# Kernel tuning notes

Hardware: AMD Instinct MI355X
Metric: run time of the kernel (lower is better)

Reference implementation:

```python
import jax, jax.numpy as jnp
import numpy as np
import math

B, T, C = 4, 2048, 1024
N = 16
D = C // N  # 64
SCALE = 1.0 / math.sqrt(C)  # weight init scale, matches 1/sqrt(in_features)


def setup_inputs() -> dict:
    key = jax.random.key(0)
    ks = jax.random.split(key, 5)
    x = jax.random.normal(ks[0], (B, T, C), dtype=jnp.float32)
    wq = jax.random.normal(ks[1], (C, C), dtype=jnp.float32) * SCALE
    wk = jax.random.normal(ks[2], (C, C), dtype=jnp.float32) * SCALE
    wv = jax.random.normal(ks[3], (C, C), dtype=jnp.float32) * SCALE
    wp = jax.random.normal(ks[4], (C, C), dtype=jnp.float32) * SCALE
    zb = jnp.zeros((C,), dtype=jnp.float32)
    return {"x": x, "wq": wq, "bq": zb, "wk": wk, "bk": zb,
            "wv": wv, "bv": zb, "wp": wp, "bp": zb}


def reference(x, wq, bq, wk, bk, wv, bv, wp, bp):
    # q/k/v projections (torch Linear: x @ W.T + b), split into heads
    q = (x @ wq.T + bq).reshape(B, T, N, D)
    k = (x @ wk.T + bk).reshape(B, T, N, D)
    v = (x @ wv.T + bv).reshape(B, T, N, D)
    # scores [B, N, T, T] with causal mask (include_query=True -> key_dim = T)
    scores = jnp.einsum('bqnd,bknd->bnqk', q, k) / math.sqrt(D)
    causal = jnp.tril(jnp.ones((T, T), dtype=bool))
    scores = jnp.where(causal[None, None], scores, -jnp.inf)
    probs = jax.nn.softmax(scores, axis=-1)
    # attention output, clamp to [-10, 10] (drop_p = 0, head_mask = None)
    attn = jnp.einsum('bnqk,bknd->bqnd', probs, v)
    attn = jnp.clip(attn, -10.0, 10.0).reshape(B, T, C)
    out = attn @ wp.T + bp
    out = jnp.clip(out, -10.0, 10.0)
    return out
```

## Files before the change

### kernel.cpp

```cpp
#include <hip/hip_runtime.h>
#include <stdint.h>

typedef __attribute__((ext_vector_type(4))) float f32x4;
typedef __attribute__((ext_vector_type(8))) _Float16 h8;
typedef __attribute__((ext_vector_type(4))) float f4v;
typedef __attribute__((ext_vector_type(4))) _Float16 h4v;

#define B_ 4
#define T_ 2048
#define C_ 1024
#define NH 16
#define HD 64
#define M_ (B_*T_)
#define KD 1024

#define MFMA16(a, b, c) __builtin_amdgcn_mfma_f32_16x16x32_f16(a, b, c, 0, 0, 0)

#if __has_builtin(__builtin_amdgcn_exp2f)
#define EXP2(x) __builtin_amdgcn_exp2f(x)
#else
#define EXP2(x) exp2f(x)
#endif

#if __has_builtin(__builtin_amdgcn_cvt_pkrtz)
static __device__ __forceinline__ unsigned pk16(float a, float b) {
  return __builtin_bit_cast(unsigned, __builtin_amdgcn_cvt_pkrtz(a, b));
}
#else
static __device__ __forceinline__ unsigned pk16(float a, float b) {
  union { _Float16 h[2]; unsigned u; } x;
  x.h[0] = (_Float16)a; x.h[1] = (_Float16)b; return x.u;
}
#endif

#define GL2LDS16(g, l) \
  __builtin_amdgcn_global_load_lds((const __attribute__((address_space(1))) unsigned int*)(g), \
      (__attribute__((address_space(3))) unsigned int*)(unsigned int)(uintptr_t)(l), 16, 0, 0)

__global__ void cast_x_kernel(const float* __restrict__ src, _Float16* __restrict__ dst, int n4) {
  int i = blockIdx.x * blockDim.x + threadIdx.x;
  if (i < n4) {
    f4v v = ((const f4v*)src)[i];
    ((h4v*)dst)[i] = __builtin_convertvector(v, h4v);
  }
}

__device__ __forceinline__ void stage_f32_128x32(const float* src, _Float16* dst, int lane, int wav) {
  #pragma unroll
  for (int hh = 0; hh < 2; hh++) {
    int row = hh*64 + wav*16 + (lane >> 2);
    int colf = (lane & 3) * 8;
    const float* p = src + (size_t)row * KD + colf;
    f4v a = *(const f4v*)p;
    f4v b = *(const f4v*)(p + 4);
    h8 v;
    v[0]=(_Float16)a[0]; v[1]=(_Float16)a[1]; v[2]=(_Float16)a[2]; v[3]=(_Float16)a[3];
    v[4]=(_Float16)b[0]; v[5]=(_Float16)b[1]; v[6]=(_Float16)b[2]; v[7]=(_Float16)b[3];
    *(h8*)(dst + row*32 + colf) = v;
  }
}

template<int AMODE>
__global__ __launch_bounds__(256) void gemm_qkv_kernel(
    const _Float16* __restrict__ Xh, const float* __restrict__ Xf,
    const float* __restrict__ Wq, const float* __restrict__ Wk, const float* __restrict__ Wv,
    const float* __restrict__ bq, const float* __restrict__ bk, const float* __restrict__ bv,
    _Float16* __restrict__ Qo, _Float16* __restrict__ Ko, _Float16* __restrict__ Vo)
{
  __shared__ _Float16 As[128*32];
  __shared__ _Float16 Bs[128*32];
  int tid = threadIdx.x;
  int lane = tid & 63, wav = tid >> 6;
  int mb = blockIdx.x;
  int nbg = blockIdx.y;
  int sel = nbg >> 3, nb = nbg & 7;
  const float* W = sel == 0 ? Wq : (sel == 1 ? Wk : Wv);
  const float* bias = sel == 0 ? bq : (sel == 1 ? bk : bv);
  _Float16* Out = sel == 0 ? Qo : (sel == 1 ? Ko : Vo);
  int m0 = mb * 128, n0 = nb * 128;

  f32x4 acc[4][4] = {};

  int r_in = lane >> 2;
  int c8   = (lane & 3) * 8;
  int l15 = lane & 15, l4 = lane >> 4;
  int wr = (wav >> 1) * 64, wc = (wav & 1) * 64;

  for (int k0 = 0; k0 < KD; k0 += 32) {
    if (AMODE == 0) {
      GL2LDS16(Xh + (size_t)(m0 +      wav*16 + r_in)*KD + k0 + c8, As +        wav*512);
      GL2LDS16(Xh + (size_t)(m0 + 64 + wav*16 + r_in)*KD + k0 + c8, As + 2048 + wav*512);
    } else {
      stage_f32_128x32(Xf + (size_t)m0 * KD + k0, As, lane, wav);
    }
    stage_f32_128x32(W + (size_t)n0 * KD + k0, Bs, lane, wav);
    __syncthreads();

    h8 af[4], bf[4];
    #pragma unroll
    for (int f = 0; f < 4; f++) {
      af[f] = *(const h8*)(As + (wr + f*16 + l15)*32 + l4*8);
      bf[f] = *(const h8*)(Bs + (wc + f*16 + l15)*32 + l4*8);
    }
    #pragma unroll
    for (int i = 0; i < 4; i++)
      #pragma unroll
      for (int j = 0; j < 4; j++)
        acc[i][j] = MFMA16(af[i], bf[j], acc[i][j]);
    __syncthreads();
  }

  if (sel == 2) {
    #pragma unroll
    for (int i = 0; i < 4; i++) {
      int mrow = m0 + wr + i*16 + l4*4;
      int bb = mrow >> 11, t = mrow & 2047;
      #pragma unroll
      for (int j = 0; j < 4; j++) {
        int ncol = n0 + wc + j*16 + l15;
        float bval = bias[ncol];
        int hh = ncol >> 6, d = ncol & 63;
        h4v v;
        #pragma unroll
        for (int r = 0; r < 4; r++) v[r] = (_Float16)(acc[i][j][r] + bval);
        *(h4v*)(Vo + ((size_t)(bb*NH + hh)*HD + d)*T_ + t) = v;
      }
    }
  } else {
    #pragma unroll
    for (int i = 0; i < 4; i++) {
      int mrow = m0 + wr + i*16 + l4*4;
      #pragma unroll
      for (int j = 0; j < 4; j++) {
        int ncol = n0 + wc + j*16 + l15;
        float bval = bias[ncol];
        #pragma unroll
        for (int r = 0; r < 4; r++)
          Out[(size_t)(mrow + r)*C_ + ncol] = (_Float16)(acc[i][j][r] + bval);
      }
    }
  }
}

__global__ __launch_bounds__(256) void gemm_proj_kernel(
    const _Float16* __restrict__ A, const float* __restrict__ W,
    const float* __restrict__ bias, float* __restrict__ Out)
{
  __shared__ _Float16 As[128*32];
  __shared__ _Float16 Bs[128*32];
  int tid = threadIdx.x;
  int lane = tid & 63, wav = tid >> 6;
  int m0 = blockIdx.x * 128, n0 = blockIdx.y * 128;

  f32x4 acc[4][4] = {};
  int r_in = lane >> 2;
  int c8   = (lane & 3) * 8;
  int l15 = lane & 15, l4 = lane >> 4;
  int wr = (wav >> 1) * 64, wc = (wav & 1) * 64;

  for (int k0 = 0; k0 < KD; k0 += 32) {
    GL2LDS16(A + (size_t)(m0 +      wav*16 + r_in)*KD + k0 + c8, As +        wav*512);
    GL2LDS16(A + (size_t)(m0 + 64 + wav*16 + r_in)*KD + k0 + c8, As + 2048 + wav*512);
    stage_f32_128x32(W + (size_t)n0 * KD + k0, Bs, lane, wav);
    __syncthreads();

    h8 af[4], bf[4];
    #pragma unroll
    for (int f = 0; f < 4; f++) {
      af[f] = *(const h8*)(As + (wr + f*16 + l15)*32 + l4*8);
      bf[f] = *(const h8*)(Bs + (wc + f*16 + l15)*32 + l4*8);
    }
    #pragma unroll
    for (int i = 0; i < 4; i++)
      #pragma unroll
      for (int j = 0; j < 4; j++)
        acc[i][j] = MFMA16(af[i], bf[j], acc[i][j]);
    __syncthreads();
  }

  #pragma unroll
  for (int i = 0; i < 4; i++) {
    int mrow = m0 + wr + i*16 + l4*4;
    #pragma unroll
    for (int j = 0; j < 4; j++) {
      int ncol = n0 + wc + j*16 + l15;
      float bval = bias[ncol];
      #pragma unroll
      for (int r = 0; r < 4; r++) {
        float v = acc[i][j][r] + bval;
        v = fminf(10.f, fmaxf(-10.f, v));
        Out[(size_t)(mrow + r)*C_ + ncol] = v;
      }
    }
  }
}

__global__ __launch_bounds__(64) void attn_kernel(
    const _Float16* Q, const _Float16* __restrict__ K,
    const _Float16* __restrict__ Vt, _Float16* O)
{
  __shared__ _Float16 Plds[2][16*72];
  int lane = threadIdx.x & 63;
  int p = blockIdx.x;
  int pair = p >> 6;
  int bh = p & 63;
  int b = bh >> 4, h = bh & 15;
  int l15 = lane & 15, l4 = lane >> 4;
  _Float16* PlA = &Plds[0][0];
  _Float16* PlB = &Plds[1][0];
  const _Float16* Kbh = K + (size_t)b*T_*C_ + h*HD;
  const _Float16* Vbh = Vt + (size_t)(b*NH + h)*HD*T_;
  const _Float16 QSC = (_Float16)0.18033688011f;

#define CHAIN(sv, qrow, m, lp, acc, Pl)                                        \
  {                                                                            \
    float sc[16];                                                              \
    _Pragma("unroll") for (int g = 0; g < 4; g++) {                            \
      sc[g*4+0] = sv[g][0]; sc[g*4+1] = sv[g][1];                              \
      sc[g*4+2] = sv[g][2]; sc[g*4+3] = sv[g][3];                              \
    }                                                                          \
    if (kb == lastb) {                                                         \
      _Pragma("unroll") for (int g = 0; g < 4; g++)                            \
        _Pragma("unroll") for (int r = 0; r < 4; r++)                          \
          if (kb + g*16 + l4*4 + r > (qrow)) sc[g*4+r] = -INFINITY;            \
    }                                                                          \
    float mx = sc[0];                                                          \
    _Pragma("unroll") for (int j = 1; j < 16; j++) mx = fmaxf(mx, sc[j]);      \
    mx = fmaxf(mx, __shfl_xor(mx, 16));                                        \
    mx = fmaxf(mx, __shfl_xor(mx, 32));                                        \
    if (__any(mx > (m) + 8.f)) {                                               \
      float mn = fmaxf((m), mx);                                               \
      float al = EXP2((m) - mn);                                               \
      (lp) *= al;                                                              \
      float av0 = __shfl(al, l4*4+0), av1 = __shfl(al, l4*4+1);                \
      float av2 = __shfl(al, l4*4+2), av3 = __shfl(al, l4*4+3);                \
      _Pragma("unroll") for (int c2 = 0; c2 < 4; c2++) {                       \
        acc[c2][0] *= av0; acc[c2][1] *= av1;                                  \
        acc[c2][2] *= av2; acc[c2][3] *= av3;                                  \
      }                                                                        \
      (m) = mn;                                                                \
    }                                                                          \
    _Pragma("unroll") for (int g = 0; g < 4; g++) {                            \
      float e0 = EXP2(sc[g*4+0] - (m)), e1 = EXP2(sc[g*4+1] - (m));            \
      float e2 = EXP2(sc[g*4+2] - (m)), e3 = EXP2(sc[g*4+3] - (m));            \
      (lp) += (e0 + e1) + (e2 + e3);                                           \
      uint2 u; u.x = pk16(e0, e1); u.y = pk16(e2, e3);                         \
      *(uint2*)((Pl) + l15*72 + g*16 + l4*4) = u;                              \
    }                                                                          \
  }

  #pragma unroll 1
  for (int ti = 0; ti < 2; ti++) {
    int t = ti ? (63 - pair) : pair;
    int q0 = t * 32;
    int qa = q0 + l15, qb = q0 + 16 + l15;

    const _Float16* qp0 = Q + (size_t)(b*T_ + qa)*C_ + h*HD;
    const _Float16* qp1 = Q + (size_t)(b*T_ + qb)*C_ + h*HD;
    h8 qf00 = *(const h8*)(qp0 + l4*8)      * QSC;
    h8 qf01 = *(const h8*)(qp0 + 32 + l4*8) * QSC;
    h8 qf10 = *(const h8*)(qp1 + l4*8)      * QSC;
    h8 qf11 = *(const h8*)(qp1 + 32 + l4*8) * QSC;

    f32x4 accA[4] = {}, accB[4] = {};
    float mA = -INFINITY, lAp = 0.f;
    float mB = -INFINITY, lBp = 0.f;
    int lastb = (q0 >> 6) << 6;

    h8 kf0, kf1, kf2, kf3, kf4, kf5, kf6, kf7;
    kf0 = *(const h8*)(Kbh + (size_t)(     l15)*C_ + l4*8);
    kf1 = *(const h8*)(Kbh + (size_t)(     l15)*C_ + 32 + l4*8);
    kf2 = *(const h8*)(Kbh + (size_t)(16 + l15)*C_ + l4*8);
    kf3 = *(const h8*)(Kbh + (size_t)(16 + l15)*C_ + 32 + l4*8);
    kf4 = *(const h8*)(Kbh + (size_t)(32 + l15)*C_ + l4*8);
    kf5 = *(const h8*)(Kbh + (size_t)(32 + l15)*C_ + 32 + l4*8);
    kf6 = *(const h8*)(Kbh + (size_t)(48 + l15)*C_ + l4*8);
    kf7 = *(const h8*)(Kbh + (size_t)(48 + l15)*C_ + 32 + l4*8);

    #pragma unroll 1
    for (int kb = 0; kb <= lastb; kb += 64) {
      h8 vf00 = *(const h8*)(Vbh + (size_t)(     l15)*T_ + kb + l4*8);
      h8 vf01 = *(const h8*)(Vbh + (size_t)(     l15)*T_ + kb + 32 + l4*8);
      h8 vf10 = *(const h8*)(Vbh + (size_t)(16 + l15)*T_ + kb + l4*8);
      h8 vf11 = *(const h8*)(Vbh + (size_t)(16 + l15)*T_ + kb + 32 + l4*8);
      h8 vf20 = *(const h8*)(Vbh + (size_t)(32 + l15)*T_ + kb + l4*8);
      h8 vf21 = *(const h8*)(Vbh + (size_t)(32 + l15)*T_ + kb + 32 + l4*8);
      h8 vf30 = *(const h8*)(Vbh + (size_t)(48 + l15)*T_ + kb + l4*8);
      h8 vf31 = *(const h8*)(Vbh + (size_t)(48 + l15)*T_ + kb + 32 + l4*8);

      f32x4 z = {};
      f32x4 sA[4], sB[4];
      sA[0] = MFMA16(kf1, qf01, MFMA16(kf0, qf00, z));
      sA[1] = MFMA16(kf3, qf01, MFMA16(kf2, qf00, z));
      sA[2] = MFMA16(kf5, qf01, MFMA16(kf4, qf00, z));
      sA[3] = MFMA16(kf7, qf01, MFMA16(kf6, qf00, z));
      sB[0] = MFMA16(kf1, qf11, MFMA16(kf0, qf10, z));
      sB[1] = MFMA16(kf3, qf11, MFMA16(kf2, qf10, z));
      sB[2] = MFMA16(kf5, qf11, MFMA16(kf4, qf10, z));
      sB[3] = MFMA16(kf7, qf11, MFMA16(kf6, qf10, z));

      if (kb < lastb) {
        const _Float16* kn = Kbh + (size_t)(kb + 64)*C_;
        kf0 = *(const h8*)(kn + (size_t)(     l15)*C_ + l4*8);
        kf1 = *(const h8*)(kn + (size_t)(     l15)*C_ + 32 + l4*8);
        kf2 = *(const h8*)(kn + (size_t)(16 + l15)*C_ + l4*8);
        kf3 = *(const h8*)(kn + (size_t)(16 + l15)*C_ + 32 + l4*8);
        kf4 = *(const h8*)(kn + (size_t)(32 + l15)*C_ + l4*8);
        kf5 = *(const h8*)(kn + (size_t)(32 + l15)*C_ + 32 + l4*8);
        kf6 = *(const h8*)(kn + (size_t)(48 + l15)*C_ + l4*8);
        kf7 = *(const h8*)(kn + (size_t)(48 + l15)*C_ + 32 + l4*8);
      }

      CHAIN(sA, qa, mA, lAp, accA, PlA)
      CHAIN(sB, qb, mB, lBp, accB, PlB)

      h8 paA0 = *(const h8*)(PlA + l15*72 + l4*8);
      h8 paA1 = *(const h8*)(PlA + l15*72 + 32 + l4*8);
      h8 paB0 = *(const h8*)(PlB + l15*72 + l4*8);
      h8 paB1 = *(const h8*)(PlB + l15*72 + 32 + l4*8);
      accA[0] = MFMA16(paA1, vf01, MFMA16(paA0, vf00, accA[0]));
      accA[1] = MFMA16(paA1, vf11, MFMA16(paA0, vf10, accA[1]));
      accA[2] = MFMA16(paA1, vf21, MFMA16(paA0, vf20, accA[2]));
      accA[3] = MFMA16(paA1, vf31, MFMA16(paA0, vf30, accA[3]));
      accB[0] = MFMA16(paB1, vf01, MFMA16(paB0, vf00, accB[0]));
      accB[1] = MFMA16(paB1, vf11, MFMA16(paB0, vf10, accB[1]));
      accB[2] = MFMA16(paB1, vf21, MFMA16(paB0, vf20, accB[2]));
      accB[3] = MFMA16(paB1, vf31, MFMA16(paB0, vf30, accB[3]));
    }

    lAp += __shfl_xor(lAp, 16); lAp += __shfl_xor(lAp, 32);
    lBp += __shfl_xor(lBp, 16); lBp += __shfl_xor(lBp, 32);
    float lrA[4], lrB[4];
    #pragma unroll
    for (int r = 0; r < 4; r++) {
      lrA[r] = 1.f / __shfl(lAp, l4*4 + r);
      lrB[r] = 1.f / __shfl(lBp, l4*4 + r);
    }
    #pragma unroll
    for (int c2 = 0; c2 < 4; c2++) {
      #pragma unroll
      for (int r = 0; r < 4; r++) {
        float va = accA[c2][r] * lrA[r];
        float vb = accB[c2][r] * lrB[r];
        va = fminf(10.f, fmaxf(-10.f, va));
        vb = fminf(10.f, fmaxf(-10.f, vb));
        O[(size_t)(b*T_ + q0      + l4*4 + r)*C_ + h*HD + c2*16 + l15] = (_Float16)va;
        O[(size_t)(b*T_ + q0 + 16 + l4*4 + r)*C_ + h*HD + c2*16 + l15] = (_Float16)vb;
      }
    }
  }
#undef CHAIN
}

extern "C" void kernel_launch(void* const* d_in, const int* in_sizes, int n_in,
                              void* d_out, int out_size, void* d_ws, size_t ws_size,
                              hipStream_t stream) {
  (void)in_sizes; (void)n_in; (void)out_size;
  const float* x  = (const float*)d_in[0];
  const float* wq = (const float*)d_in[1];
  const float* bq = (const float*)d_in[2];
  const float* wk = (const float*)d_in[3];
  const float* bk = (const float*)d_in[4];
  const float* wv = (const float*)d_in[5];
  const float* bv = (const float*)d_in[6];
  const float* wp = (const float*)d_in[7];
  const float* bp = (const float*)d_in[8];
  float* out = (float*)d_out;

  char* ws = (char*)d_ws;
  const size_t MB = 1ull << 20;
  _Float16* qh = (_Float16*)(ws + 0*MB);
  _Float16* kh = (_Float16*)(ws + 16*MB);
  _Float16* vh = (_Float16*)(ws + 32*MB);
  _Float16* xh = (_Float16*)(ws + 48*MB);

  bool use_xh = ws_size >= 64*MB;
  if (use_xh) {
    cast_x_kernel<<<dim3((M_*C_/4) / 256), 256, 0, stream>>>(x, xh, M_*C_/4);
    gemm_qkv_kernel<0><<<dim3(M_/128, 24), 256, 0, stream>>>(
        xh, nullptr, wq, wk, wv, bq, bk, bv, qh, kh, vh);
  } else {
    gemm_qkv_kernel<1><<<dim3(M_/128, 24), 256, 0, stream>>>(
        nullptr, x, wq, wk, wv, bq, bk, bv, qh, kh, vh);
  }
  attn_kernel<<<dim3(2048), 64, 0, stream>>>(qh, kh, vh, qh);
  gemm_proj_kernel<<<dim3(M_/128, C_/128), 256, 0, stream>>>(qh, wp, bp, out);
}
```

Measured before the change: 239.0 us.

## Split attention KV range across two waves per query tile with LDS merge

Replaces the one-wave block that handled a pair of causal query tiles with a two-wave block per query tile. Each wave processes half of the KV blocks, and the partial softmax states are merged through shared memory using max/sum rescaling. The grid doubles and tiles are launched in descending order of work. This aims to shorten each block's serial dependency chain and raise parallelism, at the cost of a block barrier, extra LDS traffic, and merge arithmetic. In-place writes to Q remain safe because each block reads only its own query rows.

```diff
diff --git a/kernel.cpp b/kernel.cpp
--- a/kernel.cpp
+++ b/kernel.cpp
@@ -195,22 +195,44 @@
   }
 }
 
-__global__ __launch_bounds__(64) void attn_kernel(
+__global__ __launch_bounds__(128, 4) void attn_kernel(
     const _Float16* Q, const _Float16* __restrict__ K,
     const _Float16* __restrict__ Vt, _Float16* O)
 {
-  __shared__ _Float16 Plds[2][16*72];
+  __shared__ _Float16 Plds[2][2][16*72];
+  __shared__ float MrgAcc[2][16][64];
+  __shared__ float MrgML[2][2][16];
   int lane = threadIdx.x & 63;
+  int w = threadIdx.x >> 6;
   int p = blockIdx.x;
-  int pair = p >> 6;
+  int t = 63 - (p >> 6);
   int bh = p & 63;
   int b = bh >> 4, h = bh & 15;
   int l15 = lane & 15, l4 = lane >> 4;
-  _Float16* PlA = &Plds[0][0];
-  _Float16* PlB = &Plds[1][0];
+  _Float16* PlA = &Plds[w][0][0];
+  _Float16* PlB = &Plds[w][1][0];
   const _Float16* Kbh = K + (size_t)b*T_*C_ + h*HD;
   const _Float16* Vbh = Vt + (size_t)(b*NH + h)*HD*T_;
   const _Float16 QSC = (_Float16)0.18033688011f;
+
+  int q0 = t * 32;
+  int qa = q0 + l15, qb = q0 + 16 + l15;
+  int a  = (t >> 1) + 1;
+  int h0 = (a + 1) >> 1;
+  int ibs = w ? h0 : 0;
+  int ibe = w ? a : h0;
+  int lastb = (a - 1) * 64;
+
+  const _Float16* qp0 = Q + (size_t)(b*T_ + qa)*C_ + h*HD;
+  const _Float16* qp1 = Q + (size_t)(b*T_ + qb)*C_ + h*HD;
+  h8 qf00 = *(const h8*)(qp0 + l4*8)      * QSC;
+  h8 qf01 = *(const h8*)(qp0 + 32 + l4*8) * QSC;
+  h8 qf10 = *(const h8*)(qp1 + l4*8)      * QSC;
+  h8 qf11 = *(const h8*)(qp1 + 32 + l4*8) * QSC;
+
+  f32x4 accA[4] = {}, accB[4] = {};
+  float mA = -INFINITY, lAp = 0.f;
+  float mB = -INFINITY, lBp = 0.f;
 
 #define CHAIN(sv, qrow, m, lp, acc, Pl)                                        \
   {                                                                            \
@@ -249,107 +271,115 @@
     }                                                                          \
   }
 
+  h8 kf0, kf1, kf2, kf3, kf4, kf5, kf6, kf7;
+  {
+    const _Float16* k0p = Kbh + (size_t)(ibs * 64) * C_;
+    kf0 = *(const h8*)(k0p + (size_t)(     l15)*C_ + l4*8);
+    kf1 = *(const h8*)(k0p + (size_t)(     l15)*C_ + 32 + l4*8);
+    kf2 = *(const h8*)(k0p + (size_t)(16 + l15)*C_ + l4*8);
+    kf3 = *(const h8*)(k0p + (size_t)(16 + l15)*C_ + 32 + l4*8);
+    kf4 = *(const h8*)(k0p + (size_t)(32 + l15)*C_ + l4*8);
+    kf5 = *(const h8*)(k0p + (size_t)(32 + l15)*C_ + 32 + l4*8);
+    kf6 = *(const h8*)(k0p + (size_t)(48 + l15)*C_ + l4*8);
+    kf7 = *(const h8*)(k0p + (size_t)(48 + l15)*C_ + 32 + l4*8);
+  }
+
   #pragma unroll 1
-  for (int ti = 0; ti < 2; ti++) {
-    int t = ti ? (63 - pair) : pair;
-    int q0 = t * 32;
-    int qa = q0 + l15, qb = q0 + 16 + l15;
-
-    const _Float16* qp0 = Q + (size_t)(b*T_ + qa)*C_ + h*HD;
-    const _Float16* qp1 = Q + (size_t)(b*T_ + qb)*C_ + h*HD;
-    h8 qf00 = *(const h8*)(qp0 + l4*8)      * QSC;
-    h8 qf01 = *(const h8*)(qp0 + 32 + l4*8) * QSC;
-    h8 qf10 = *(const h8*)(qp1 + l4*8)      * QSC;
-    h8 qf11 = *(const h8*)(qp1 + 32 + l4*8) * QSC;
-
-    f32x4 accA[4] = {}, accB[4] = {};
-    float mA = -INFINITY, lAp = 0.f;
-    float mB = -INFINITY, lBp = 0.f;
-    int lastb = (q0 >> 6) << 6;
-
-    h8 kf0, kf1, kf2, kf3, kf4, kf5, kf6, kf7;
-    kf0 = *(const h8*)(Kbh + (size_t)(     l15)*C_ + l4*8);
-    kf1 = *(const h8*)(Kbh + (size_t)(     l15)*C_ + 32 + l4*8);
-    kf2 = *(const h8*)(Kbh + (size_t)(16 + l15)*C_ + l4*8);
-    kf3 = *(const h8*)(Kbh + (size_t)(16 + l15)*C_ + 32 + l4*8);
-    kf4 = *(const h8*)(Kbh + (size_t)(32 + l15)*C_ + l4*8);
-    kf5 = *(const h8*)(Kbh + (size_t)(32 + l15)*C_ + 32 + l4*8);
-    kf6 = *(const h8*)(Kbh + (size_t)(48 + l15)*C_ + l4*8);
-    kf7 = *(const h8*)(Kbh + (size_t)(48 + l15)*C_ + 32 + l4*8);
-
-    #pragma unroll 1
-    for (int kb = 0; kb <= lastb; kb += 64) {
-      h8 vf00 = *(const h8*)(Vbh + (size_t)(     l15)*T_ + kb + l4*8);
-      h8 vf01 = *(const h8*)(Vbh + (size_t)(     l15)*T_ + kb + 32 + l4*8);
-      h8 vf10 = *(const h8*)(Vbh + (size_t)(16 + l15)*T_ + kb + l4*8);
-      h8 vf11 = *(const h8*)(Vbh + (size_t)(16 + l15)*T_ + kb + 32 + l4*8);
-      h8 vf20 = *(const h8*)(Vbh + (size_t)(32 + l15)*T_ + kb + l4*8);
-      h8 vf21 = *(const h8*)(Vbh + (size_t)(32 + l15)*T_ + kb + 32 + l4*8);
-      h8 vf30 = *(const h8*)(Vbh + (size_t)(48 + l15)*T_ + kb + l4*8);
-      h8 vf31 = *(const h8*)(Vbh + (size_t)(48 + l15)*T_ + kb + 32 + l4*8);
-
-      f32x4 z = {};
-      f32x4 sA[4], sB[4];
-      sA[0] = MFMA16(kf1, qf01, MFMA16(kf0, qf00, z));
-      sA[1] = MFMA16(kf3, qf01, MFMA16(kf2, qf00, z));
-      sA[2] = MFMA16(kf5, qf01, MFMA16(kf4, qf00, z));
-      sA[3] = MFMA16(kf7, qf01, MFMA16(kf6, qf00, z));
-      sB[0] = MFMA16(kf1, qf11, MFMA16(kf0, qf10, z));
-      sB[1] = MFMA16(kf3, qf11, MFMA16(kf2, qf10, z));
-      sB[2] = MFMA16(kf5, qf11, MFMA16(kf4, qf10, z));
-      sB[3] = MFMA16(kf7, qf11, MFMA16(kf6, qf10, z));
-
-      if (kb < lastb) {
-        const _Float16* kn = Kbh + (size_t)(kb + 64)*C_;
-        kf0 = *(const h8*)(kn + (size_t)(     l15)*C_ + l4*8);
-        kf1 = *(const h8*)(kn + (size_t)(     l15)*C_ + 32 + l4*8);
-        kf2 = *(const h8*)(kn + (size_t)(16 + l15)*C_ + l4*8);
-        kf3 = *(const h8*)(kn + (size_t)(16 + l15)*C_ + 32 + l4*8);
-        kf4 = *(const h8*)(kn + (size_t)(32 + l15)*C_ + l4*8);
-        kf5 = *(const h8*)(kn + (size_t)(32 + l15)*C_ + 32 + l4*8);
-        kf6 = *(const h8*)(kn + (size_t)(48 + l15)*C_ + l4*8);
-        kf7 = *(const h8*)(kn + (size_t)(48 + l15)*C_ + 32 + l4*8);
+  for (int ib = ibs; ib < ibe; ib++) {
+    int kb = ib << 6;
+    h8 vf00 = *(const h8*)(Vbh + (size_t)(     l15)*T_ + kb + l4*8);
+    h8 vf01 = *(const h8*)(Vbh + (size_t)(     l15)*T_ + kb + 32 + l4*8);
+    h8 vf10 = *(const h8*)(Vbh + (size_t)(16 + l15)*T_ + kb + l4*8);
+    h8 vf11 = *(const h8*)(Vbh + (size_t)(16 + l15)*T_ + kb + 32 + l4*8);
+    h8 vf20 = *(const h8*)(Vbh + (size_t)(32 + l15)*T_ + kb + l4*8);
+    h8 vf21 = *(const h8*)(Vbh + (size_t)(32 + l15)*T_ + kb + 32 + l4*8);
+    h8 vf30 = *(const h8*)(Vbh + (size_t)(48 + l15)*T_ + kb + l4*8);
+    h8 vf31 = *(const h8*)(Vbh + (size_t)(48 + l15)*T_ + kb + 32 + l4*8);
+
+    f32x4 z = {};
+    f32x4 sA[4], sB[4];
+    sA[0] = MFMA16(kf1, qf01, MFMA16(kf0, qf00, z));
+    sA[1] = MFMA16(kf3, qf01, MFMA16(kf2, qf00, z));
+    sA[2] = MFMA16(kf5, qf01, MFMA16(kf4, qf00, z));
+    sA[3] = MFMA16(kf7, qf01, MFMA16(kf6, qf00, z));
+    sB[0] = MFMA16(kf1, qf11, MFMA16(kf0, qf10, z));
+    sB[1] = MFMA16(kf3, qf11, MFMA16(kf2, qf10, z));
+    sB[2] = MFMA16(kf5, qf11, MFMA16(kf4, qf10, z));
+    sB[3] = MFMA16(kf7, qf11, MFMA16(kf6, qf10, z));
+
+    if (ib + 1 < ibe) {
+      const _Float16* kn = Kbh + (size_t)(kb + 64)*C_;
+      kf0 = *(const h8*)(kn + (size_t)(     l15)*C_ + l4*8);
+      kf1 = *(const h8*)(kn + (size_t)(     l15)*C_ + 32 + l4*8);
+      kf2 = *(const h8*)(kn + (size_t)(16 + l15)*C_ + l4*8);
+      kf3 = *(const h8*)(kn + (size_t)(16 + l15)*C_ + 32 + l4*8);
+      kf4 = *(const h8*)(kn + (size_t)(32 + l15)*C_ + l4*8);
+      kf5 = *(const h8*)(kn + (size_t)(32 + l15)*C_ + 32 + l4*8);
+      kf6 = *(const h8*)(kn + (size_t)(48 + l15)*C_ + l4*8);
+      kf7 = *(const h8*)(kn + (size_t)(48 + l15)*C_ + 32 + l4*8);
+    }
+
+    CHAIN(sA, qa, mA, lAp, accA, PlA)
+    CHAIN(sB, qb, mB, lBp, accB, PlB)
+
+    h8 paA0 = *(const h8*)(PlA + l15*72 + l4*8);
+    h8 paA1 = *(const h8*)(PlA + l15*72 + 32 + l4*8);
+    h8 paB0 = *(const h8*)(PlB + l15*72 + l4*8);
+    h8 paB1 = *(const h8*)(PlB + l15*72 + 32 + l4*8);
+    accA[0] = MFMA16(paA1, vf01, MFMA16(paA0, vf00, accA[0]));
+    accA[1] = MFMA16(paA1, vf11, MFMA16(paA0, vf10, accA[1]));
+    accA[2] = MFMA16(paA1, vf21, MFMA16(paA0, vf20, accA[2]));
+    accA[3] = MFMA16(paA1, vf31, MFMA16(paA0, vf30, accA[3]));
+    accB[0] = MFMA16(paB1, vf01, MFMA16(paB0, vf00, accB[0]));
+    accB[1] = MFMA16(paB1, vf11, MFMA16(paB0, vf10, accB[1]));
+    accB[2] = MFMA16(paB1, vf21, MFMA16(paB0, vf20, accB[2]));
+    accB[3] = MFMA16(paB1, vf31, MFMA16(paB0, vf30, accB[3]));
+  }
+#undef CHAIN
+
+  lAp += __shfl_xor(lAp, 16); lAp += __shfl_xor(lAp, 32);
+  lBp += __shfl_xor(lBp, 16); lBp += __shfl_xor(lBp, 32);
+
+  if (w == 1) {
+    if (l4 == 0) {
+      MrgML[0][0][l15] = mA; MrgML[0][1][l15] = lAp;
+      MrgML[1][0][l15] = mB; MrgML[1][1][l15] = lBp;
+    }
+    #pragma unroll
+    for (int c2 = 0; c2 < 4; c2++)
+      #pragma unroll
+      for (int r = 0; r < 4; r++) {
+        MrgAcc[0][l4*4 + r][c2*16 + l15] = accA[c2][r];
+        MrgAcc[1][l4*4 + r][c2*16 + l15] = accB[c2][r];
       }
-
-      CHAIN(sA, qa, mA, lAp, accA, PlA)
-      CHAIN(sB, qb, mB, lBp, accB, PlB)
-
-      h8 paA0 = *(const h8*)(PlA + l15*72 + l4*8);
-      h8 paA1 = *(const h8*)(PlA + l15*72 + 32 + l4*8);
-      h8 paB0 = *(const h8*)(PlB + l15*72 + l4*8);
-      h8 paB1 = *(const h8*)(PlB + l15*72 + 32 + l4*8);
-      accA[0] = MFMA16(paA1, vf01, MFMA16(paA0, vf00, accA[0]));
-      accA[1] = MFMA16(paA1, vf11, MFMA16(paA0, vf10, accA[1]));
-      accA[2] = MFMA16(paA1, vf21, MFMA16(paA0, vf20, accA[2]));
-      accA[3] = MFMA16(paA1, vf31, MFMA16(paA0, vf30, accA[3]));
-      accB[0] = MFMA16(paB1, vf01, MFMA16(paB0, vf00, accB[0]));
-      accB[1] = MFMA16(paB1, vf11, MFMA16(paB0, vf10, accB[1]));
-      accB[2] = MFMA16(paB1, vf21, MFMA16(paB0, vf20, accB[2]));
-      accB[3] = MFMA16(paB1, vf31, MFMA16(paB0, vf30, accB[3]));
-    }
-
-    lAp += __shfl_xor(lAp, 16); lAp += __shfl_xor(lAp, 32);
-    lBp += __shfl_xor(lBp, 16); lBp += __shfl_xor(lBp, 32);
-    float lrA[4], lrB[4];
+  }
+  __syncthreads();
+  if (w == 0) {
     #pragma unroll
     for (int r = 0; r < 4; r++) {
-      lrA[r] = 1.f / __shfl(lAp, l4*4 + r);
-      lrB[r] = 1.f / __shfl(lBp, l4*4 + r);
-    }
-    #pragma unroll
-    for (int c2 = 0; c2 < 4; c2++) {
-      #pragma unroll
-      for (int r = 0; r < 4; r++) {
-        float va = accA[c2][r] * lrA[r];
-        float vb = accB[c2][r] * lrB[r];
+      int row = l4*4 + r;
+      float m0a = __shfl(mA, row), l0a = __shfl(lAp, row);
+      float m0b = __shfl(mB, row), l0b = __shfl(lBp, row);
+      float m1a = MrgML[0][0][row], l1a = MrgML[0][1][row];
+      float m1b = MrgML[1][0][row], l1b = MrgML[1][1][row];
+      float msa = fmaxf(m0a, m1a), msb = fmaxf(m0b, m1b);
+      float w0a = EXP2(m0a - msa), w1a = EXP2(m1a - msa);
+      float w0b = EXP2(m0b - msb), w1b = EXP2(m1b - msb);
+      float ra = 1.f / (w0a*l0a + w1a*l1a);
+      float rb = 1.f / (w0b*l0b + w1b*l1b);
+      float s0a = w0a*ra, s1a = w1a*ra;
+      float s0b = w0b*rb, s1b = w1b*rb;
+      #pragma unroll
+      for (int c2 = 0; c2 < 4; c2++) {
+        float va = accA[c2][r]*s0a + MrgAcc[0][row][c2*16 + l15]*s1a;
+        float vb = accB[c2][r]*s0b + MrgAcc[1][row][c2*16 + l15]*s1b;
         va = fminf(10.f, fmaxf(-10.f, va));
         vb = fminf(10.f, fmaxf(-10.f, vb));
-        O[(size_t)(b*T_ + q0      + l4*4 + r)*C_ + h*HD + c2*16 + l15] = (_Float16)va;
-        O[(size_t)(b*T_ + q0 + 16 + l4*4 + r)*C_ + h*HD + c2*16 + l15] = (_Float16)vb;
+        O[(size_t)(b*T_ + q0      + row)*C_ + h*HD + c2*16 + l15] = (_Float16)va;
+        O[(size_t)(b*T_ + q0 + 16 + row)*C_ + h*HD + c2*16 + l15] = (_Float16)vb;
       }
     }
   }
-#undef CHAIN
 }
 
 extern "C" void kernel_launch(void* const* d_in, const int* in_sizes, int n_in,
@@ -383,6 +413,6 @@
     gemm_qkv_kernel<1><<<dim3(M_/128, 24), 256, 0, stream>>>(
         nullptr, x, wq, wk, wv, bq, bk, bv, qh, kh, vh);
   }
-  attn_kernel<<<dim3(2048), 64, 0, stream>>>(qh, kh, vh, qh);
+  attn_kernel<<<dim3(4096), 128, 0, stream>>>(qh, kh, vh, qh);
   gemm_proj_kernel<<<dim3(M_/128, C_/128), 256, 0, stream>>>(qh, wp, bp, out);
 }
```

Result: slower. 459.4 us (+92.2%).
